# Optimization experiments

Hardware: AMD Instinct MI355X
Metric: run time of the kernel (lower is better)

Reference implementation:

```python
import jax, jax.numpy as jnp
import numpy as np
from jax import lax

HID = 256
CB_N = 512   # codebook_size
CB_D = 64    # codebook_dim
FC = 6       # force_channels
COMMIT_W = 0.25


def _conv(x, w, b, stride):
    # x: [B,C,H,W], w: [O,I,3,3], 'same'-style padding=1
    y = lax.conv_general_dilated(x, w, (stride, stride), ((1, 1), (1, 1)),
                                 dimension_numbers=('NCHW', 'OIHW', 'NCHW'))
    return y + b[None, :, None, None]


def _silu(x):
    return x * jax.nn.sigmoid(x)


def setup_inputs() -> dict:
    key = jax.random.key(0)
    ks = jax.random.split(key, 8)
    s = 0.05
    force_field = jax.random.normal(ks[0], (8, FC, 256, 256), dtype=jnp.float32)
    w1 = jax.random.normal(ks[1], (HID, FC, 3, 3), dtype=jnp.float32) * s
    b1 = jnp.zeros((HID,), dtype=jnp.float32)
    w2 = jax.random.normal(ks[2], (HID, HID, 3, 3), dtype=jnp.float32) * s
    b2 = jnp.zeros((HID,), dtype=jnp.float32)
    w3 = jax.random.normal(ks[3], (CB_D, HID, 3, 3), dtype=jnp.float32) * s
    b3 = jnp.zeros((CB_D,), dtype=jnp.float32)
    codebook = jax.random.uniform(ks[4], (CB_N, CB_D), dtype=jnp.float32,
                                  minval=-1.0 / CB_N, maxval=1.0 / CB_N)
    return {"force_field": force_field, "w1": w1, "b1": b1, "w2": w2,
            "b2": b2, "w3": w3, "b3": b3, "codebook": codebook}


def reference(force_field, w1, b1, w2, b2, w3, b3, codebook):
    # Encoder: conv(pad1) -> SiLU -> conv(stride2) -> SiLU -> conv(stride2)
    h = _silu(_conv(force_field, w1, b1, 1))
    h = _silu(_conv(h, w2, b2, 2))
    z = _conv(h, w3, b3, 2)                      # [B, CB_D, h, w]
    B, C, hh, ww = z.shape
    z_flat = jnp.transpose(z, (0, 2, 3, 1)).reshape(-1, C)  # [N, CB_D]
    # pairwise squared distances: ||z||^2 + ||c||^2 - 2 z.c
    dists = (jnp.sum(z_flat * z_flat, axis=1, keepdims=True)
             + jnp.sum(codebook * codebook, axis=1)
             - 2.0 * (z_flat @ codebook.T))      # [N, CB_N]
    indices = jnp.argmin(dists, axis=1)          # [N] int
    z_q = codebook[indices].reshape(B, hh, ww, C).transpose(0, 3, 1, 2)
    commitment_loss = (jnp.mean((lax.stop_gradient(z_q) - z) ** 2)
                       + COMMIT_W * jnp.mean((z_q - lax.stop_gradient(z)) ** 2))
    tokens = indices.reshape(B, hh, ww)
    return tokens, commitment_loss
```

## Files before the change

### kernel.cpp

```cpp
#include <hip/hip_runtime.h>
#include <math.h>


#define FC    6
#define HID   256
#define CB_N  512
#define CB_D  64

typedef _Float16 f16x8 __attribute__((ext_vector_type(8)));
typedef _Float16 f16x4 __attribute__((ext_vector_type(4)));
typedef float f32x16 __attribute__((ext_vector_type(16)));

#define H1N_IMG    17105920
#define H2N_IMG    4359168

#define FFP_ROW    260
#define FFP_CI     (258 * FFP_ROW)
#define FFP_IMG    (6 * FFP_CI)

__global__ void fill_sentinel_kernel(float* out, int n) {
    int i = blockIdx.x * 256 + threadIdx.x;
    if (i < n) out[i] = -12345.0f;
}

__global__ void h1n_guard_kernel(unsigned int* h1n, int nslots) {
    int i = blockIdx.x * 256 + threadIdx.x;
    if (i >= nslots * 132096) return;
    int slot = i / 132096;
    int r    = i - slot * 132096;
    unsigned int* base = h1n + (size_t)slot * H1N_IMG;
    if (r < 66560) base[r] = 0u;
    else {
        int r2  = r - 66560;
        int j   = r2 & 3;
        int hl  = (r2 >> 2) & 1;
        int cg  = (r2 >> 3) & 31;
        int row = (r2 >> 8) + 1;
        base[(size_t)row * 66560 + 33280 + cg * 1040 + hl * 520 + j] = 0u;
    }
}

__global__ void h2n_guard_kernel(unsigned int* h2n, int nslots) {
    int i = blockIdx.x * 256 + threadIdx.x;
    if (i >= nslots * 66560) return;
    int slot = i / 66560;
    int r    = i - slot * 66560;
    unsigned int* base = h2n + (size_t)slot * H2N_IMG;
    if (r < 33792) base[r] = 0u;
    else {
        int r2  = r - 33792;
        int j   = r2 & 3;
        int hl  = (r2 >> 2) & 1;
        int cg  = (r2 >> 3) & 31;
        int row = (r2 >> 8) + 1;
        base[(size_t)row * 33792 + 16896 + cg * 528 + hl * 264 + j] = 0u;
    }
}

__global__ void wswz1_kernel(const float* __restrict__ w1, _Float16* __restrict__ wsz) {
    int i = blockIdx.x * 256 + threadIdx.x;
    if (i >= 2 * 4 * 4096) return;
    int j   = i & 7;
    int co_ = (i >> 3) & 127;
    int kc  = (i >> 10) & 1;
    int hf  = (i >> 11) & 1;
    int st  = (i >> 12) & 3;
    int ct  = i >> 14;
    int k   = st * 16 + kc * 8 + j;
    int co  = ct * 128 + co_;
    float v = (k < 54) ? w1[(size_t)co * 54 + k] : 0.f;
    _Float16 h = (_Float16)v;
    _Float16 l = (_Float16)(v - (float)h);
    wsz[i] = hf ? l : h;
}

__global__ void wswz2_kernel(const float* __restrict__ w2, _Float16* __restrict__ wsz) {
    int i = blockIdx.x * 256 + threadIdx.x;
    if (i >= 2 * 144 * 4096) return;
    int j   = i & 7;
    int co_ = (i >> 3) & 127;
    int kc  = (i >> 10) & 1;
    int hf  = (i >> 11) & 1;
    int st  = (i >> 12) % 144;
    int ct  = (i >> 12) / 144;
    int r    = st / 48;
    int kq   = st - r * 48;
    int kc16 = kq / 3;
    int s    = kq - kc16 * 3;
    int ci   = kc16 * 16 + kc * 8 + j;
    int rs   = r * 3 + s;
    float v = w2[(size_t)(ct * 128 + co_) * 2304 + ci * 9 + rs];
    _Float16 h = (_Float16)v;
    _Float16 l = (_Float16)(v - (float)h);
    wsz[i] = hf ? l : h;
}

__global__ void wswz3_kernel(const float* __restrict__ w3, _Float16* __restrict__ wsz) {
    int i = blockIdx.x * 256 + threadIdx.x;
    if (i >= 144 * 2048) return;
    int j  = i & 7;
    int co = (i >> 3) & 63;
    int kc = (i >> 9) & 1;
    int hf = (i >> 10) & 1;
    int st = i >> 11;
    int ci = (st & 15) * 16 + kc * 8 + j;
    int rs = st >> 4;
    float v = w3[(size_t)co * 2304 + ci * 9 + rs];
    _Float16 h = (_Float16)v;
    _Float16 l = (_Float16)(v - (float)h);
    wsz[i] = hf ? l : h;
}

__global__ void cnorm_kernel(const float* __restrict__ cb, float* __restrict__ cn) {
    int j = blockIdx.x * 256 + threadIdx.x;
    if (j < CB_N) {
        const float* p = cb + j * CB_D;
        float s0 = 0.f, s1 = 0.f, s2 = 0.f, s3 = 0.f;
        for (int i = 0; i < CB_D; i += 4) {
            s0 = fmaf(p[i],   p[i],   s0);
            s1 = fmaf(p[i+1], p[i+1], s1);
            s2 = fmaf(p[i+2], p[i+2], s2);
            s3 = fmaf(p[i+3], p[i+3], s3);
        }
        cn[j] = (s0 + s1) + (s2 + s3);
    }
}

__device__ __forceinline__ float silu_f(float v) {
    return v / (1.f + expf(-v));
}

__device__ __forceinline__ unsigned int pack_hl(float v) {
    _Float16 h = (_Float16)v;
    _Float16 l = (_Float16)(v - (float)h);
    unsigned short hb = __builtin_bit_cast(unsigned short, h);
    unsigned short lb = __builtin_bit_cast(unsigned short, l);
    return (unsigned int)hb | ((unsigned int)lb << 16);
}

__device__ __forceinline__ f16x8 as_f16x8(uint4 v) {
    return __builtin_bit_cast(f16x8, v);
}

__device__ __forceinline__ unsigned int ldu32_sb(const char* base, unsigned off, int px) {
    return *(const unsigned int*)(base + (unsigned)__builtin_amdgcn_readfirstlane((int)off) + px * 4);
}

__device__ __forceinline__ void sync_lds() {
    asm volatile("s_waitcnt lgkmcnt(0)\n\ts_barrier" ::: "memory");
}

__global__ __launch_bounds__(256) void ffpack_kernel(const float* __restrict__ ff,
                                                     unsigned int* __restrict__ ffp) {
    const int gw   = (blockIdx.x * 256 + threadIdx.x) >> 6;
    const int lane = threadIdx.x & 63;
    const int y  = gw & 255;
    const int ic = gw >> 8;
    const float* rowp = ff + ((size_t)ic * 256 + y) * 256;
    float4 v = *(const float4*)(rowp + 4 * lane);
    unsigned p0 = pack_hl(v.x), p1 = pack_hl(v.y), p2 = pack_hl(v.z), p3 = pack_hl(v.w);
    unsigned p3p = __shfl_up(p3, 1);
    if (lane == 0) p3p = 0u;
    unsigned int* orow = ffp + ((size_t)ic * 258 + y + 1) * FFP_ROW;
    uint4 o; o.x = p3p; o.y = p0; o.z = p1; o.w = p2;
    *(uint4*)(orow + 4 * lane) = o;
    if (lane == 63) { orow[256] = p3; orow[257] = 0u; }
}

__global__ __launch_bounds__(256) void conv1_mfma_kernel(
        const unsigned int* __restrict__ ffp,
        const _Float16* __restrict__ wsz1,
        const float* __restrict__ bias,
        unsigned int* __restrict__ h1n,
        int b0) {
    __shared__ __align__(16) _Float16 ldsA[2][2][128][8];
    __shared__ __align__(16) _Float16 ldsB[2][128][24];
    __shared__ __align__(16) unsigned int T[64];
    __shared__ float biasl[128];

    const int tid = threadIdx.x;
    const int py  = blockIdx.x >> 1;
    const int xt  = blockIdx.x & 1;
    const int ct  = blockIdx.y;
    const int img = blockIdx.z;

    const unsigned int* ffpi = ffp + (size_t)(b0 + img) * FFP_IMG;
    _Float16* h1f = (_Float16*)(h1n + (size_t)img * H1N_IMG);

    if (tid < 64) {
        int k = tid;
        unsigned off;
        if (k < 54) {
            int ci  = k / 9;
            int tap = k - ci * 9;
            int r   = tap / 3;
            int s   = tap - r * 3;
            off = (unsigned)((((size_t)ci * 258 + py + r) * FFP_ROW + xt * 128 + s) * 4);
        } else {
            off = (unsigned)((xt * 128) * 4);
        }
        T[k] = off;
    }
    if (tid < 128) biasl[tid] = bias[ct * 128 + tid];
    __syncthreads();

    const int lane = tid & 63;
    const int w    = tid >> 6;
    const int cow  = (w >> 1) * 64;
    const int pxw  = (w & 1) * 64;
    const int m_   = lane & 31;
    const int kc   = lane >> 5;
    const int px   = tid & 127;
    const int kh   = tid >> 7;

    f32x16 acc[2][2];
    #pragma unroll
    for (int a = 0; a < 2; a++)
        #pragma unroll
        for (int b = 0; b < 2; b++)
            #pragma unroll
            for (int r = 0; r < 16; r++) acc[a][b][r] = 0.f;

    uint4* aldsf = (uint4*)&ldsA[0][0][0][0];
    const char* gbase = (const char*)ffpi;

    uint4 a0, a1;
    unsigned v0, v1, v2, v3, v4, v5, v6, v7;
    {
        const uint4* ag = (const uint4*)(wsz1 + ((size_t)(ct * 4)) * 4096);
        a0 = ag[tid];
        a1 = ag[tid + 256];
        const int k0 = kh * 8;
        uint4 rb0 = *(const uint4*)&T[k0];
        uint4 rb1 = *(const uint4*)&T[k0 + 4];
        v0 = ldu32_sb(gbase, rb0.x, px); v1 = ldu32_sb(gbase, rb0.y, px);
        v2 = ldu32_sb(gbase, rb0.z, px); v3 = ldu32_sb(gbase, rb0.w, px);
        v4 = ldu32_sb(gbase, rb1.x, px); v5 = ldu32_sb(gbase, rb1.y, px);
        v6 = ldu32_sb(gbase, rb1.z, px); v7 = ldu32_sb(gbase, rb1.w, px);
    }

    for (int t = 0; t < 4; t++) {
        sync_lds();

        aldsf[tid]       = a0;
        aldsf[tid + 256] = a1;
        uint4 bh, bl;
        bh.x = (v0 & 0xffffu) | (v1 << 16);
        bh.y = (v2 & 0xffffu) | (v3 << 16);
        bh.z = (v4 & 0xffffu) | (v5 << 16);
        bh.w = (v6 & 0xffffu) | (v7 << 16);
        bl.x = (v0 >> 16) | (v1 & 0xffff0000u);
        bl.y = (v2 >> 16) | (v3 & 0xffff0000u);
        bl.z = (v4 >> 16) | (v5 & 0xffff0000u);
        bl.w = (v6 >> 16) | (v7 & 0xffff0000u);
        *(uint4*)&ldsB[0][px][kh * 8] = bh;
        *(uint4*)&ldsB[1][px][kh * 8] = bl;

        sync_lds();

        if (t < 3) {
            const uint4* ag = (const uint4*)(wsz1 + ((size_t)(ct * 4 + t + 1)) * 4096);
            a0 = ag[tid];
            a1 = ag[tid + 256];
            const int k0 = (t + 1) * 16 + kh * 8;
            uint4 rb0 = *(const uint4*)&T[k0 & 63];
            uint4 rb1 = *(const uint4*)&T[(k0 + 4) & 63];
            v0 = ldu32_sb(gbase, rb0.x, px); v1 = ldu32_sb(gbase, rb0.y, px);
            v2 = ldu32_sb(gbase, rb0.z, px); v3 = ldu32_sb(gbase, rb0.w, px);
            v4 = ldu32_sb(gbase, rb1.x, px); v5 = ldu32_sb(gbase, rb1.y, px);
            v6 = ldu32_sb(gbase, rb1.z, px); v7 = ldu32_sb(gbase, rb1.w, px);
        }

        f16x8 ah0 = *(const f16x8*)&ldsA[0][kc][cow + m_][0];
        f16x8 ah1 = *(const f16x8*)&ldsA[0][kc][cow + 32 + m_][0];
        f16x8 al0 = *(const f16x8*)&ldsA[1][kc][cow + m_][0];
        f16x8 al1 = *(const f16x8*)&ldsA[1][kc][cow + 32 + m_][0];
        f16x8 xh0 = *(const f16x8*)&ldsB[0][pxw + m_][kc * 8];
        f16x8 xh1 = *(const f16x8*)&ldsB[0][pxw + 32 + m_][kc * 8];
        f16x8 xl0 = *(const f16x8*)&ldsB[1][pxw + m_][kc * 8];
        f16x8 xl1 = *(const f16x8*)&ldsB[1][pxw + 32 + m_][kc * 8];

        acc[0][0] = __builtin_amdgcn_mfma_f32_32x32x16_f16(ah0, xh0, acc[0][0], 0, 0, 0);
        acc[0][1] = __builtin_amdgcn_mfma_f32_32x32x16_f16(ah0, xh1, acc[0][1], 0, 0, 0);
        acc[1][0] = __builtin_amdgcn_mfma_f32_32x32x16_f16(ah1, xh0, acc[1][0], 0, 0, 0);
        acc[1][1] = __builtin_amdgcn_mfma_f32_32x32x16_f16(ah1, xh1, acc[1][1], 0, 0, 0);
        acc[0][0] = __builtin_amdgcn_mfma_f32_32x32x16_f16(ah0, xl0, acc[0][0], 0, 0, 0);
        acc[0][1] = __builtin_amdgcn_mfma_f32_32x32x16_f16(ah0, xl1, acc[0][1], 0, 0, 0);
        acc[1][0] = __builtin_amdgcn_mfma_f32_32x32x16_f16(ah1, xl0, acc[1][0], 0, 0, 0);
        acc[1][1] = __builtin_amdgcn_mfma_f32_32x32x16_f16(ah1, xl1, acc[1][1], 0, 0, 0);
        acc[0][0] = __builtin_amdgcn_mfma_f32_32x32x16_f16(al0, xh0, acc[0][0], 0, 0, 0);
        acc[0][1] = __builtin_amdgcn_mfma_f32_32x32x16_f16(al0, xh1, acc[0][1], 0, 0, 0);
        acc[1][0] = __builtin_amdgcn_mfma_f32_32x32x16_f16(al1, xh0, acc[1][0], 0, 0, 0);
        acc[1][1] = __builtin_amdgcn_mfma_f32_32x32x16_f16(al1, xh1, acc[1][1], 0, 0, 0);
    }

    #pragma unroll
    for (int mt = 0; mt < 2; mt++) {
        #pragma unroll
        for (int nt = 0; nt < 2; nt++) {
            const int pxo = xt * 128 + pxw + nt * 32 + m_;
            const int par = pxo & 1;
            const int xs  = par ? ((pxo + 1) >> 1) : (pxo >> 1);
            _Float16* dst = h1f + (size_t)(py + 1) * 133120 + par * 66560 + xs * 8 + kc * 4;
            #pragma unroll
            for (int q = 0; q < 4; q++) {
                const int cb_ = cow + mt * 32 + 8 * q + 4 * kc;
                const int cg  = (ct * 128 + cow + mt * 32 + 8 * q) >> 3;
                f16x4 oh, ol;
                #pragma unroll
                for (int j = 0; j < 4; j++) {
                    float v = silu_f(acc[mt][nt][4*q+j] + biasl[cb_ + j]);
                    _Float16 h = (_Float16)v;
                    oh[j] = h;
                    ol[j] = (_Float16)(v - (float)h);
                }
                *(f16x4*)(dst + (size_t)cg * 2080)        = oh;
                *(f16x4*)(dst + (size_t)cg * 2080 + 1040) = ol;
            }
        }
    }
}

__global__ __launch_bounds__(256, 4) void conv2_mfma_kernel(
        const unsigned int* __restrict__ h1n,
        const _Float16* __restrict__ wsz2,
        const float* __restrict__ bias,
        unsigned int* __restrict__ h2n) {
    __shared__ __align__(16) char ldsB[2 * 8192];
    __shared__ float biasl[128];

    const int tid = threadIdx.x;
    const int py  = blockIdx.x >> 1;
    const int xt  = blockIdx.x & 1;
    const int ct  = blockIdx.y;
    const int img = blockIdx.z;

    if (tid < 128) biasl[tid] = bias[ct * 128 + tid];

    const int lane = tid & 63;
    const int w    = tid >> 6;
    const int cow  = (w >> 1) * 64;
    const int pxw  = (w & 1) * 32;
    const int m_   = lane & 31;
    const int kc   = lane >> 5;

    const char* bbase = (const char*)(h1n + (size_t)img * H1N_IMG);
    const char* abase = (const char*)wsz2 + (size_t)ct * 144 * 8192
                        + (size_t)kc * 2048 + (size_t)(cow + m_) * 16;

    const int spx = tid & 63;
    const int skc = (tid >> 6) & 1;
    const int shl = tid >> 7;
    const unsigned sgfix = (unsigned)(skc * 4160 + spx * 16 + xt * 1024 + shl * 2080);
    const unsigned swfix = (unsigned)(shl * 2048 + skc * 1024 + spx * 16);
    const unsigned rfix0 = (unsigned)(kc * 1024 + (pxw + m_) * 16);

    auto offu = [&](int t) -> unsigned {
        int r    = t / 48;
        int kq   = t - r * 48;
        int kc16 = kq / 3;
        int s    = kq - kc16 * 3;
        return (unsigned)((2 * py + r) * 266240 + (s != 1 ? 133120 : 0)
                          + (s == 2 ? 16 : 0) + kc16 * 8320);
    };

    f32x16 acc[2];
    #pragma unroll
    for (int a = 0; a < 2; a++)
        #pragma unroll
        for (int r = 0; r < 16; r++) acc[a][r] = 0.f;

    uint4 pa0, pa1, pa2, pa3;
    uint4 wa0, wa1;
    uint4 wb0, wb1;
    {
        pa0 = *(const uint4*)(abase);
        pa1 = *(const uint4*)(abase + 512);
        pa2 = *(const uint4*)(abase + 4096);
        pa3 = *(const uint4*)(abase + 4096 + 512);
        uint4 t0v = *(const uint4*)(bbase + offu(0) + sgfix);
        *(uint4*)(ldsB + swfix) = t0v;
        uint4 t1v = *(const uint4*)(bbase + offu(1) + sgfix);
        *(uint4*)(ldsB + 4096 + swfix) = t1v;
        wa0 = *(const uint4*)(bbase + offu(2) + sgfix);
        wa1 = *(const uint4*)(bbase + offu(3) + sgfix);
        wb0 = *(const uint4*)(bbase + offu(4) + sgfix);
        wb1 = *(const uint4*)(bbase + offu(5) + sgfix);
    }
    sync_lds();

    auto superstep = [&](int s, uint4& W0, uint4& W1) {
        const int t0 = 2 * s;
        char* rslot = ldsB + (s & 1) * 8192;

        if (s < 71) {
            char* wslot = ldsB + ((s + 1) & 1) * 8192;
            *(uint4*)(wslot + swfix)        = W0;
            *(uint4*)(wslot + 4096 + swfix) = W1;
        }

        f16x8 xh0 = *(const f16x8*)(rslot + rfix0);
        f16x8 xl0 = *(const f16x8*)(rslot + 2048 + rfix0);

        uint4 ca0 = pa0, ca1 = pa1, ca2 = pa2, ca3 = pa3;
        {
            const char* ap = abase + (size_t)(t0 + 1) * 8192;
            pa0 = *(const uint4*)(ap);
            pa1 = *(const uint4*)(ap + 512);
            pa2 = *(const uint4*)(ap + 4096);
            pa3 = *(const uint4*)(ap + 4096 + 512);
        }

        f16x8 ah0 = as_f16x8(ca0);
        f16x8 ah1 = as_f16x8(ca1);
        f16x8 al0 = as_f16x8(ca2);
        f16x8 al1 = as_f16x8(ca3);

        acc[0] = __builtin_amdgcn_mfma_f32_32x32x16_f16(ah0, xh0, acc[0], 0, 0, 0);
        acc[1] = __builtin_amdgcn_mfma_f32_32x32x16_f16(ah1, xh0, acc[1], 0, 0, 0);
        acc[0] = __builtin_amdgcn_mfma_f32_32x32x16_f16(ah0, xl0, acc[0], 0, 0, 0);
        acc[1] = __builtin_amdgcn_mfma_f32_32x32x16_f16(ah1, xl0, acc[1], 0, 0, 0);
        acc[0] = __builtin_amdgcn_mfma_f32_32x32x16_f16(al0, xh0, acc[0], 0, 0, 0);
        acc[1] = __builtin_amdgcn_mfma_f32_32x32x16_f16(al1, xh0, acc[1], 0, 0, 0);

        f16x8 yh0 = *(const f16x8*)(rslot + 4096 + rfix0);
        f16x8 yl0 = *(const f16x8*)(rslot + 6144 + rfix0);

        ca0 = pa0; ca1 = pa1; ca2 = pa2; ca3 = pa3;
        if (s < 71) {
            const char* ap = abase + (size_t)(t0 + 2) * 8192;
            pa0 = *(const uint4*)(ap);
            pa1 = *(const uint4*)(ap + 512);
            pa2 = *(const uint4*)(ap + 4096);
            pa3 = *(const uint4*)(ap + 4096 + 512);
        }

        ah0 = as_f16x8(ca0);
        ah1 = as_f16x8(ca1);
        al0 = as_f16x8(ca2);
        al1 = as_f16x8(ca3);

        acc[0] = __builtin_amdgcn_mfma_f32_32x32x16_f16(ah0, yh0, acc[0], 0, 0, 0);
        acc[1] = __builtin_amdgcn_mfma_f32_32x32x16_f16(ah1, yh0, acc[1], 0, 0, 0);
        acc[0] = __builtin_amdgcn_mfma_f32_32x32x16_f16(ah0, yl0, acc[0], 0, 0, 0);
        acc[1] = __builtin_amdgcn_mfma_f32_32x32x16_f16(ah1, yl0, acc[1], 0, 0, 0);
        acc[0] = __builtin_amdgcn_mfma_f32_32x32x16_f16(al0, yh0, acc[0], 0, 0, 0);
        acc[1] = __builtin_amdgcn_mfma_f32_32x32x16_f16(al1, yh0, acc[1], 0, 0, 0);

        if (s < 69) {
            W0 = *(const uint4*)(bbase + offu(t0 + 6) + sgfix);
            W1 = *(const uint4*)(bbase + offu(t0 + 7) + sgfix);
        }

        sync_lds();
    };

    for (int ss = 0; ss < 36; ss++) {
        superstep(2 * ss,     wa0, wa1);
        superstep(2 * ss + 1, wb0, wb1);
    }

    _Float16* h2f = (_Float16*)(h2n + (size_t)img * H2N_IMG);
    const int pxo = xt * 64 + pxw + m_;
    const int par = pxo & 1;
    const int xs  = par ? ((pxo + 1) >> 1) : (pxo >> 1);
    _Float16* dst = h2f + (size_t)(py + 1) * 67584 + par * 33792 + xs * 8 + kc * 4;
    #pragma unroll
    for (int mt = 0; mt < 2; mt++) {
        #pragma unroll
        for (int q = 0; q < 4; q++) {
            const int cb_ = cow + mt * 32 + 8 * q + 4 * kc;
            const int cg  = (ct * 128 + cow + mt * 32 + 8 * q) >> 3;
            f16x4 oh, ol;
            #pragma unroll
            for (int j = 0; j < 4; j++) {
                float v = silu_f(acc[mt][4*q+j] + biasl[cb_ + j]);
                _Float16 h = (_Float16)v;
                oh[j] = h;
                ol[j] = (_Float16)(v - (float)h);
            }
            *(f16x4*)(dst + (size_t)cg * 1056)       = oh;
            *(f16x4*)(dst + (size_t)cg * 1056 + 528) = ol;
        }
    }
}

__global__ __launch_bounds__(64) void conv3_mfma_kernel(
        const unsigned int* __restrict__ h2n,
        const _Float16* __restrict__ wsz3,
        const float* __restrict__ bias,
        float* __restrict__ z) {
    const int bi  = blockIdx.x;
    const int img = blockIdx.y;
    const int py  = bi >> 2;
    const int ct3 = (bi >> 1) & 1;
    const int pxt = bi & 1;

    const int lane = threadIdx.x;
    const int m_   = lane & 31;
    const int kc   = lane >> 5;

    const char* bbase = (const char*)(h2n + (size_t)img * H2N_IMG);
    const char* abase = (const char*)wsz3 + (size_t)kc * 1024 + (size_t)(ct3 * 32 + m_) * 16;
    const unsigned bfix = (unsigned)(kc * 2112 + (pxt * 32 + m_) * 16);

    auto offu = [&](int t) -> unsigned {
        int rs = t >> 4;
        int r  = (rs * 11) >> 5;
        int s  = rs - 3 * r;
        return (unsigned)((2 * py + r) * 135168 + (s != 1 ? 67584 : 0)
                          + (s == 2 ? 16 : 0) + (t & 15) * 4224);
    };

    f32x16 acc;
    #pragma unroll
    for (int r = 0; r < 16; r++) acc[r] = 0.f;

    uint4 rh[8], rl[8];
    #pragma unroll
    for (int i = 0; i < 8; i++) {
        unsigned o = offu(i);
        rh[i] = *(const uint4*)(bbase + o + bfix);
        rl[i] = *(const uint4*)(bbase + o + bfix + 1056);
    }
    uint4 pa0 = *(const uint4*)(abase);
    uint4 pa1 = *(const uint4*)(abase + 2048);

    for (int tb = 0; tb < 144; tb += 8) {
        #pragma unroll
        for (int i = 0; i < 8; i++) {
            const int t = tb + i;
            uint4 cbh = rh[i], cbl = rl[i];
            if (t + 8 < 144) {
                unsigned o = offu(t + 8);
                rh[i] = *(const uint4*)(bbase + o + bfix);
                rl[i] = *(const uint4*)(bbase + o + bfix + 1056);
            }
            uint4 ca0 = pa0, ca1 = pa1;
            if (t < 143) {
                const char* ap = abase + (size_t)(t + 1) * 4096;
                pa0 = *(const uint4*)(ap);
                pa1 = *(const uint4*)(ap + 2048);
            }
            f16x8 ah = as_f16x8(ca0);
            f16x8 al = as_f16x8(ca1);
            f16x8 xh = as_f16x8(cbh);
            f16x8 xl = as_f16x8(cbl);
            acc = __builtin_amdgcn_mfma_f32_32x32x16_f16(ah, xh, acc, 0, 0, 0);
            acc = __builtin_amdgcn_mfma_f32_32x32x16_f16(ah, xl, acc, 0, 0, 0);
            acc = __builtin_amdgcn_mfma_f32_32x32x16_f16(al, xh, acc, 0, 0, 0);
        }
    }

    const int x = pxt * 32 + m_;
    float* zp = z + (((size_t)img * 64 + py) * 64 + x) * 64;
    #pragma unroll
    for (int q = 0; q < 4; q++) {
        const int co = ct3 * 32 + 8 * q + 4 * kc;
        float4 o;
        o.x = acc[4*q+0] + bias[co + 0];
        o.y = acc[4*q+1] + bias[co + 1];
        o.z = acc[4*q+2] + bias[co + 2];
        o.w = acc[4*q+3] + bias[co + 3];
        *(float4*)(zp + co) = o;
    }
}

__global__ __launch_bounds__(128) void vqpart_kernel(const float* __restrict__ z,
                                                     const float* __restrict__ cb,
                                                     const float* __restrict__ cn,
                                                     float* __restrict__ part_d,
                                                     int* __restrict__ part_i) {
    __shared__ __align__(16) float lds_cb[128 * 64];
    __shared__ float lds_cn[128];

    const int tid = threadIdx.x;
    const int q   = blockIdx.y;
    const int n   = blockIdx.x * 128 + tid;

    #pragma unroll
    for (int i = 0; i < 16; i++) {
        const int f4 = tid + 128 * i;
        *(float4*)&lds_cb[f4 * 4] = *(const float4*)(cb + q * 8192 + f4 * 4);
    }
    lds_cn[tid] = cn[q * 128 + tid];
    __syncthreads();

    float zr[64];
    const float* zp = z + (size_t)n * 64;
    #pragma unroll
    for (int i = 0; i < 16; i++)
        *(float4*)&zr[i * 4] = *(const float4*)(zp + i * 4);

    float zn0 = 0.f, zn1 = 0.f, zn2 = 0.f, zn3 = 0.f;
    #pragma unroll
    for (int i = 0; i < 64; i += 4) {
        zn0 = fmaf(zr[i],   zr[i],   zn0);
        zn1 = fmaf(zr[i+1], zr[i+1], zn1);
        zn2 = fmaf(zr[i+2], zr[i+2], zn2);
        zn3 = fmaf(zr[i+3], zr[i+3], zn3);
    }
    const float znorm = (zn0 + zn1) + (zn2 + zn3);

    float dmin = 1e30f;
    int best = 0;
    for (int j = 0; j < 128; j++) {
        const float* cp = &lds_cb[j * 64];
        float d0 = 0.f, d1 = 0.f, d2 = 0.f, d3 = 0.f;
        #pragma unroll
        for (int i = 0; i < 16; i++) {
            const float4 c4 = *(const float4*)&cp[i * 4];
            d0 = fmaf(zr[i*4],   c4.x, d0);
            d1 = fmaf(zr[i*4+1], c4.y, d1);
            d2 = fmaf(zr[i*4+2], c4.z, d2);
            d3 = fmaf(zr[i*4+3], c4.w, d3);
        }
        const float dot = (d0 + d1) + (d2 + d3);
        const float d = (znorm + lds_cn[j]) - 2.f * dot;
        if (d < dmin) { dmin = d; best = q * 128 + j; }
    }

    part_d[(size_t)q * 32768 + n] = dmin;
    part_i[(size_t)q * 32768 + n] = best;
}

__global__ __launch_bounds__(256) void vqred_kernel(const float* __restrict__ z,
                                                    const float* __restrict__ cb,
                                                    const float* __restrict__ part_d,
                                                    const int* __restrict__ part_i,
                                                    float* __restrict__ tokens_out,
                                                    float* __restrict__ loss_accum) {
    __shared__ float red[4];
    const int tid = threadIdx.x;
    const int n   = blockIdx.x * 256 + tid;

    float dmin = part_d[n];
    int   best = part_i[n];
    #pragma unroll
    for (int q = 1; q < 4; q++) {
        float d = part_d[(size_t)q * 32768 + n];
        int   i = part_i[(size_t)q * 32768 + n];
        if (d < dmin) { dmin = d; best = i; }
    }
    tokens_out[n] = (float)best;

    float zr[64];
    const float* zp = z + (size_t)n * 64;
    #pragma unroll
    for (int i = 0; i < 16; i++)
        *(float4*)&zr[i * 4] = *(const float4*)(zp + i * 4);

    const float* cbest = cb + (size_t)best * 64;
    float l0 = 0.f, l1 = 0.f, l2 = 0.f, l3 = 0.f;
    #pragma unroll
    for (int i = 0; i < 64; i += 4) {
        float t0 = cbest[i]     - zr[i];
        float t1 = cbest[i + 1] - zr[i + 1];
        float t2 = cbest[i + 2] - zr[i + 2];
        float t3 = cbest[i + 3] - zr[i + 3];
        l0 = fmaf(t0, t0, l0);
        l1 = fmaf(t1, t1, l1);
        l2 = fmaf(t2, t2, l2);
        l3 = fmaf(t3, t3, l3);
    }
    float l = (l0 + l1) + (l2 + l3);
    #pragma unroll
    for (int off = 32; off > 0; off >>= 1)
        l += __shfl_down(l, off);
    if ((tid & 63) == 0) red[tid >> 6] = l;
    __syncthreads();
    if (tid == 0)
        atomicAdd(loss_accum, (red[0] + red[1]) + (red[2] + red[3]));
}

__global__ void finalize_kernel(const float* __restrict__ loss_accum,
                                float* __restrict__ out_loss) {
    const float m = loss_accum[0] / 2097152.f;
    out_loss[0] = m + 0.25f * m;
}

extern "C" void kernel_launch(void* const* d_in, const int* in_sizes, int n_in,
                              void* d_out, int out_size, void* d_ws, size_t ws_size,
                              hipStream_t stream) {
    const float* ff = (const float*)d_in[0];
    const float* w1 = (const float*)d_in[1];
    const float* b1 = (const float*)d_in[2];
    const float* w2 = (const float*)d_in[3];
    const float* b2 = (const float*)d_in[4];
    const float* w3 = (const float*)d_in[5];
    const float* b3 = (const float*)d_in[6];
    const float* cb = (const float*)d_in[7];
    float* out = (float*)d_out;
    float* ws  = (float*)d_ws;

    const size_t TAIL = 2097152 + 8 * (size_t)FFP_IMG + 589824 + 147456 + 16384
                      + 512 + 131072 + 131072 + 1;
    auto need_u32 = [&](int nimg) -> size_t {
        return (size_t)nimg * (H1N_IMG + H2N_IMG) + TAIL;
    };

    int nimg;
    if      (ws_size >= need_u32(8) * 4) nimg = 8;
    else if (ws_size >= need_u32(4) * 4) nimg = 4;
    else if (ws_size >= need_u32(2) * 4) nimg = 2;
    else {
        fill_sentinel_kernel<<<(out_size + 255) / 256, 256, 0, stream>>>(out, out_size);
        return;
    }

    unsigned int* h1n  = (unsigned int*)ws;
    unsigned int* h2n  = h1n + (size_t)nimg * H1N_IMG;
    float*        zbuf = (float*)(h2n + (size_t)nimg * H2N_IMG);
    unsigned int* ffp  = (unsigned int*)(zbuf + 2097152);
    _Float16* wsz2 = (_Float16*)(ffp + 8 * (size_t)FFP_IMG);
    _Float16* wsz3 = wsz2 + 1179648;
    _Float16* wsz1 = wsz3 + 294912;
    float*    cn   = (float*)(wsz1 + 32768);
    float*    pd   = cn + 512;
    int*      pi   = (int*)(pd + 131072);
    float*    lacc = (float*)(pi + 131072);

    hipMemsetAsync(ffp, 0, 8 * (size_t)FFP_IMG * 4, stream);
    h1n_guard_kernel<<<(nimg * 132096 + 255) / 256, 256, 0, stream>>>(h1n, nimg);
    h2n_guard_kernel<<<(nimg * 66560 + 255) / 256, 256, 0, stream>>>(h2n, nimg);
    wswz1_kernel<<<(2 * 4 * 4096 + 255) / 256, 256, 0, stream>>>(w1, wsz1);
    wswz2_kernel<<<(2 * 144 * 4096 + 255) / 256, 256, 0, stream>>>(w2, wsz2);
    wswz3_kernel<<<(144 * 2048 + 255) / 256, 256, 0, stream>>>(w3, wsz3);
    cnorm_kernel<<<2, 256, 0, stream>>>(cb, cn);
    ffpack_kernel<<<3072, 256, 0, stream>>>(ff, ffp);

    for (int b0 = 0; b0 < 8; b0 += nimg) {
        conv1_mfma_kernel<<<dim3(512, 2, nimg), 256, 0, stream>>>(ffp, wsz1, b1, h1n, b0);
        conv2_mfma_kernel<<<dim3(256, 2, nimg), 256, 0, stream>>>(h1n, wsz2, b2, h2n);
        conv3_mfma_kernel<<<dim3(256, nimg), 64, 0, stream>>>(
            h2n, wsz3, b3, zbuf + (size_t)b0 * 262144);
    }

    hipMemsetAsync(lacc, 0, sizeof(float), stream);
    vqpart_kernel<<<dim3(256, 4), 128, 0, stream>>>(zbuf, cb, cn, pd, pi);
    vqred_kernel<<<128, 256, 0, stream>>>(zbuf, cb, pd, pi, out, lacc);
    finalize_kernel<<<1, 1, 0, stream>>>(lacc, out + 32768);
}
```

Before: 974.7 us.

## Load conv2 activation fragments directly from global, dropping LDS staging and barriers

```diff
diff --git a/kernel.cpp b/kernel.cpp
--- a/kernel.cpp
+++ b/kernel.cpp
@@ -326,16 +326,11 @@
         const _Float16* __restrict__ wsz2,
         const float* __restrict__ bias,
         unsigned int* __restrict__ h2n) {
-    __shared__ __align__(16) char ldsB[2 * 8192];
-    __shared__ float biasl[128];
-
     const int tid = threadIdx.x;
     const int py  = blockIdx.x >> 1;
     const int xt  = blockIdx.x & 1;
     const int ct  = blockIdx.y;
     const int img = blockIdx.z;
-
-    if (tid < 128) biasl[tid] = bias[ct * 128 + tid];
 
     const int lane = tid & 63;
     const int w    = tid >> 6;
@@ -344,16 +339,10 @@
     const int m_   = lane & 31;
     const int kc   = lane >> 5;
 
-    const char* bbase = (const char*)(h1n + (size_t)img * H1N_IMG);
+    const char* bbase = (const char*)(h1n + (size_t)img * H1N_IMG)
+                        + (size_t)kc * 4160 + (size_t)(xt * 64 + pxw + m_) * 16;
     const char* abase = (const char*)wsz2 + (size_t)ct * 144 * 8192
                         + (size_t)kc * 2048 + (size_t)(cow + m_) * 16;
-
-    const int spx = tid & 63;
-    const int skc = (tid >> 6) & 1;
-    const int shl = tid >> 7;
-    const unsigned sgfix = (unsigned)(skc * 4160 + spx * 16 + xt * 1024 + shl * 2080);
-    const unsigned swfix = (unsigned)(shl * 2048 + skc * 1024 + spx * 16);
-    const unsigned rfix0 = (unsigned)(kc * 1024 + (pxw + m_) * 16);
 
     auto offu = [&](int t) -> unsigned {
         int r    = t / 48;
@@ -370,96 +359,53 @@
         #pragma unroll
         for (int r = 0; r < 16; r++) acc[a][r] = 0.f;
 
-    uint4 pa0, pa1, pa2, pa3;
-    uint4 wa0, wa1;
-    uint4 wb0, wb1;
-    {
-        pa0 = *(const uint4*)(abase);
-        pa1 = *(const uint4*)(abase + 512);
-        pa2 = *(const uint4*)(abase + 4096);
-        pa3 = *(const uint4*)(abase + 4096 + 512);
-        uint4 t0v = *(const uint4*)(bbase + offu(0) + sgfix);
-        *(uint4*)(ldsB + swfix) = t0v;
-        uint4 t1v = *(const uint4*)(bbase + offu(1) + sgfix);
-        *(uint4*)(ldsB + 4096 + swfix) = t1v;
-        wa0 = *(const uint4*)(bbase + offu(2) + sgfix);
-        wa1 = *(const uint4*)(bbase + offu(3) + sgfix);
-        wb0 = *(const uint4*)(bbase + offu(4) + sgfix);
-        wb1 = *(const uint4*)(bbase + offu(5) + sgfix);
-    }
-    sync_lds();
-
-    auto superstep = [&](int s, uint4& W0, uint4& W1) {
-        const int t0 = 2 * s;
-        char* rslot = ldsB + (s & 1) * 8192;
-
-        if (s < 71) {
-            char* wslot = ldsB + ((s + 1) & 1) * 8192;
-            *(uint4*)(wslot + swfix)        = W0;
-            *(uint4*)(wslot + 4096 + swfix) = W1;
-        }
-
-        f16x8 xh0 = *(const f16x8*)(rslot + rfix0);
-        f16x8 xl0 = *(const f16x8*)(rslot + 2048 + rfix0);
-
-        uint4 ca0 = pa0, ca1 = pa1, ca2 = pa2, ca3 = pa3;
-        {
-            const char* ap = abase + (size_t)(t0 + 1) * 8192;
-            pa0 = *(const uint4*)(ap);
-            pa1 = *(const uint4*)(ap + 512);
-            pa2 = *(const uint4*)(ap + 4096);
-            pa3 = *(const uint4*)(ap + 4096 + 512);
-        }
-
-        f16x8 ah0 = as_f16x8(ca0);
-        f16x8 ah1 = as_f16x8(ca1);
-        f16x8 al0 = as_f16x8(ca2);
-        f16x8 al1 = as_f16x8(ca3);
-
-        acc[0] = __builtin_amdgcn_mfma_f32_32x32x16_f16(ah0, xh0, acc[0], 0, 0, 0);
-        acc[1] = __builtin_amdgcn_mfma_f32_32x32x16_f16(ah1, xh0, acc[1], 0, 0, 0);
-        acc[0] = __builtin_amdgcn_mfma_f32_32x32x16_f16(ah0, xl0, acc[0], 0, 0, 0);
-        acc[1] = __builtin_amdgcn_mfma_f32_32x32x16_f16(ah1, xl0, acc[1], 0, 0, 0);
-        acc[0] = __builtin_amdgcn_mfma_f32_32x32x16_f16(al0, xh0, acc[0], 0, 0, 0);
-        acc[1] = __builtin_amdgcn_mfma_f32_32x32x16_f16(al1, xh0, acc[1], 0, 0, 0);
-
-        f16x8 yh0 = *(const f16x8*)(rslot + 4096 + rfix0);
-        f16x8 yl0 = *(const f16x8*)(rslot + 6144 + rfix0);
-
-        ca0 = pa0; ca1 = pa1; ca2 = pa2; ca3 = pa3;
-        if (s < 71) {
-            const char* ap = abase + (size_t)(t0 + 2) * 8192;
-            pa0 = *(const uint4*)(ap);
-            pa1 = *(const uint4*)(ap + 512);
-            pa2 = *(const uint4*)(ap + 4096);
-            pa3 = *(const uint4*)(ap + 4096 + 512);
-        }
-
-        ah0 = as_f16x8(ca0);
-        ah1 = as_f16x8(ca1);
-        al0 = as_f16x8(ca2);
-        al1 = as_f16x8(ca3);
-
-        acc[0] = __builtin_amdgcn_mfma_f32_32x32x16_f16(ah0, yh0, acc[0], 0, 0, 0);
-        acc[1] = __builtin_amdgcn_mfma_f32_32x32x16_f16(ah1, yh0, acc[1], 0, 0, 0);
-        acc[0] = __builtin_amdgcn_mfma_f32_32x32x16_f16(ah0, yl0, acc[0], 0, 0, 0);
-        acc[1] = __builtin_amdgcn_mfma_f32_32x32x16_f16(ah1, yl0, acc[1], 0, 0, 0);
-        acc[0] = __builtin_amdgcn_mfma_f32_32x32x16_f16(al0, yh0, acc[0], 0, 0, 0);
-        acc[1] = __builtin_amdgcn_mfma_f32_32x32x16_f16(al1, yh0, acc[1], 0, 0, 0);
-
-        if (s < 69) {
-            W0 = *(const uint4*)(bbase + offu(t0 + 6) + sgfix);
-            W1 = *(const uint4*)(bbase + offu(t0 + 7) + sgfix);
-        }
-
-        sync_lds();
-    };
-
-    for (int ss = 0; ss < 36; ss++) {
-        superstep(2 * ss,     wa0, wa1);
-        superstep(2 * ss + 1, wb0, wb1);
-    }
-
+    uint4 rbh[4], rbl[4];
+    #pragma unroll
+    for (int i = 0; i < 4; i++) {
+        unsigned o = offu(i);
+        rbh[i] = *(const uint4*)(bbase + o);
+        rbl[i] = *(const uint4*)(bbase + o + 2080);
+    }
+    uint4 pa0 = *(const uint4*)(abase);
+    uint4 pa1 = *(const uint4*)(abase + 512);
+    uint4 pa2 = *(const uint4*)(abase + 4096);
+    uint4 pa3 = *(const uint4*)(abase + 4096 + 512);
+
+    for (int tb = 0; tb < 144; tb += 4) {
+        #pragma unroll
+        for (int i = 0; i < 4; i++) {
+            const int t = tb + i;
+            uint4 cbh = rbh[i], cbl = rbl[i];
+            if (t + 4 < 144) {
+                unsigned o = offu(t + 4);
+                rbh[i] = *(const uint4*)(bbase + o);
+                rbl[i] = *(const uint4*)(bbase + o + 2080);
+            }
+            uint4 ca0 = pa0, ca1 = pa1, ca2 = pa2, ca3 = pa3;
+            if (t < 143) {
+                const char* ap = abase + (size_t)(t + 1) * 8192;
+                pa0 = *(const uint4*)(ap);
+                pa1 = *(const uint4*)(ap + 512);
+                pa2 = *(const uint4*)(ap + 4096);
+                pa3 = *(const uint4*)(ap + 4096 + 512);
+            }
+            f16x8 ah0 = as_f16x8(ca0);
+            f16x8 ah1 = as_f16x8(ca1);
+            f16x8 al0 = as_f16x8(ca2);
+            f16x8 al1 = as_f16x8(ca3);
+            f16x8 xh  = as_f16x8(cbh);
+            f16x8 xl  = as_f16x8(cbl);
+
+            acc[0] = __builtin_amdgcn_mfma_f32_32x32x16_f16(ah0, xh, acc[0], 0, 0, 0);
+            acc[1] = __builtin_amdgcn_mfma_f32_32x32x16_f16(ah1, xh, acc[1], 0, 0, 0);
+            acc[0] = __builtin_amdgcn_mfma_f32_32x32x16_f16(ah0, xl, acc[0], 0, 0, 0);
+            acc[1] = __builtin_amdgcn_mfma_f32_32x32x16_f16(ah1, xl, acc[1], 0, 0, 0);
+            acc[0] = __builtin_amdgcn_mfma_f32_32x32x16_f16(al0, xh, acc[0], 0, 0, 0);
+            acc[1] = __builtin_amdgcn_mfma_f32_32x32x16_f16(al1, xh, acc[1], 0, 0, 0);
+        }
+    }
+
+    const float* bp = bias + ct * 128;
     _Float16* h2f = (_Float16*)(h2n + (size_t)img * H2N_IMG);
     const int pxo = xt * 64 + pxw + m_;
     const int par = pxo & 1;
@@ -474,7 +420,7 @@
             f16x4 oh, ol;
             #pragma unroll
             for (int j = 0; j < 4; j++) {
-                float v = silu_f(acc[mt][4*q+j] + biasl[cb_ + j]);
+                float v = silu_f(acc[mt][4*q+j] + bp[cb_ + j]);
                 _Float16 h = (_Float16)v;
                 oh[j] = h;
                 ol[j] = (_Float16)(v - (float)h);
```

Measured after the change: 1.027 ms. 1.05x slower.
